# Kernel optimization log

Hardware: AMD Instinct MI355X
Metric: run time of the kernel (lower is better)

The kernel has to match this reference:

```python
import jax, jax.numpy as jnp
from jax import lax
import numpy as np
import math

D_MODEL = 1024
D_STATE = 16
DT_RANK = 64  # ceil(1024/16)


def setup_inputs() -> dict:
    key = jax.random.key(0)
    ks = jax.random.split(key, 8)
    B, L = 2, 2048
    x = jax.random.normal(ks[0], (B, L, D_MODEL), dtype=jnp.float32)
    A_log = jnp.full((D_MODEL, D_STATE), math.log(0.5), dtype=jnp.float32)
    x_proj_w = jax.random.normal(ks[1], (DT_RANK + 2 * D_STATE, D_MODEL), dtype=jnp.float32) * (D_MODEL ** -0.5)
    dt_init_std = DT_RANK ** -0.5
    dt_proj_w = jax.random.uniform(ks[2], (D_MODEL, DT_RANK), minval=-dt_init_std, maxval=dt_init_std, dtype=jnp.float32)
    # dt bias init: softplus-inverse of dt sampled log-uniform in [2*dt_min, 2*dt_max] (trend)
    dt = jnp.exp(jax.random.uniform(ks[3], (D_MODEL,), dtype=jnp.float32) * (math.log(0.2) - math.log(0.002)) + math.log(0.002))
    dt = jnp.clip(dt, 1e-4)
    dt_proj_b = dt + jnp.log(-jnp.expm1(-dt))
    D_param = jnp.ones((D_MODEL,), dtype=jnp.float32)
    trend_emphasis = jnp.full((D_MODEL,), 0.1, dtype=jnp.float32)
    return {
        "x": x, "A_log": A_log, "x_proj_w": x_proj_w,
        "dt_proj_w": dt_proj_w, "dt_proj_b": dt_proj_b,
        "D_param": D_param, "trend_emphasis": trend_emphasis,
    }


def _selective_scan(u, delta, A, Bp, Cp, D_param):
    # u, delta: [B,L,D]; A: [D,N]; Bp, Cp: [B,L,N]; D_param: [D]
    deltaA = jnp.exp(jnp.einsum('bld,dn->bldn', delta, A))       # [B,L,D,N]
    deltaBu = jnp.einsum('bld,bln->bldn', delta * u, Bp)          # [B,L,D,N]
    Bsz, L, Dm, N = deltaA.shape

    def step(h, inp):
        dA, dBu, c = inp          # dA,dBu: [B,D,N]; c: [B,N]
        h = dA * h + dBu
        y = jnp.einsum('bdn,bn->bd', h, c)
        return h, y

    h0 = jnp.zeros((Bsz, Dm, N), dtype=u.dtype)
    xs = (jnp.moveaxis(deltaA, 1, 0), jnp.moveaxis(deltaBu, 1, 0), jnp.moveaxis(Cp, 1, 0))
    _, ys = lax.scan(step, h0, xs)            # ys: [L,B,D]
    y = jnp.moveaxis(ys, 0, 1)                # [B,L,D]
    return y + u * D_param


def reference(x, A_log, x_proj_w, dt_proj_w, dt_proj_b, D_param, trend_emphasis):
    # trend component: channel-wise emphasis gate (dropout in eval mode = identity)
    x = x * jax.nn.sigmoid(trend_emphasis)
    xz = x @ x_proj_w.T                                  # [B,L,dt_rank+2N]
    delta_part = xz[..., :DT_RANK]
    Bp = xz[..., DT_RANK:DT_RANK + D_STATE]              # [B,L,N]
    Cp = xz[..., DT_RANK + D_STATE:]                     # [B,L,N]
    delta = jax.nn.softplus(delta_part @ dt_proj_w.T + dt_proj_b)  # [B,L,D]
    A = -jnp.exp(A_log.astype(jnp.float32))
    return _selective_scan(x, delta, A, Bp, Cp, D_param.astype(jnp.float32))
```

## Files before the change

### kernel.cpp

```cpp
#include <hip/hip_runtime.h>
#include <math.h>


#define LOG2E 1.44269504088896340736f
typedef float v2f __attribute__((ext_vector_type(2)));

__device__ __forceinline__ float fexp2(float v){
#if defined(__has_builtin)
#if __has_builtin(__builtin_amdgcn_exp2f)
  return __builtin_amdgcn_exp2f(v);
#else
  return exp2f(v);
#endif
#else
  return exp2f(v);
#endif
}

__device__ __forceinline__ float fsoftplus(float v){
  return fmaxf(v, 0.f) + __logf(1.f + __expf(-fabsf(v)));
}

__global__ __launch_bounds__(256) void k_prep(const float* __restrict__ xpw,
                                              const float* __restrict__ dtw,
                                              const float* __restrict__ alog,
                                              const float* __restrict__ te,
                                              float* __restrict__ w2T,
                                              float* __restrict__ dtwT,
                                              float* __restrict__ A2,
                                              float* __restrict__ sg){
  __shared__ float sm[32 * 33];
  const int bid = blockIdx.x, t = threadIdx.x;
  const int lane = t & 31, srow = t >> 5;
  if (bid < 96){
    const int kt = bid / 3, ct = bid - kt * 3;
#pragma unroll
    for (int r = 0; r < 4; r++){
      const int cr = srow * 4 + r;
      sm[cr * 33 + lane] = xpw[(size_t)(ct * 32 + cr) * 1024 + kt * 32 + lane];
    }
    __syncthreads();
#pragma unroll
    for (int r = 0; r < 4; r++){
      const int kr = srow * 4 + r;
      const int kg = kt * 32 + kr;
      const float s = 1.f / (1.f + __expf(-te[kg]));
      w2T[(size_t)kg * 96 + ct * 32 + lane] = sm[lane * 33 + kr] * s;
    }
  } else if (bid < 160){
    const int idx = bid - 96, dti = idx >> 1, kt2 = idx & 1;
#pragma unroll
    for (int r = 0; r < 4; r++){
      const int cr = srow * 4 + r;
      sm[cr * 33 + lane] = dtw[(size_t)(dti * 32 + cr) * 64 + kt2 * 32 + lane];
    }
    __syncthreads();
#pragma unroll
    for (int r = 0; r < 4; r++){
      const int kr = srow * 4 + r;
      dtwT[(size_t)(kt2 * 32 + kr) * 1024 + dti * 32 + lane] = sm[lane * 33 + kr];
    }
  } else if (bid < 176){
    const int j = (bid - 160) * 1024 + t;
#pragma unroll
    for (int i = 0; i < 4; i++)
      A2[j + i * 256] = -__expf(alog[j + i * 256]) * LOG2E;
  } else {
#pragma unroll
    for (int i = 0; i < 4; i++){
      const int m = i * 256 + t;
      sg[m] = 1.f / (1.f + __expf(-te[m]));
    }
  }
}

__global__ __launch_bounds__(256) void k_xz(const float* __restrict__ x,
                                            const float* __restrict__ w2T,
                                            float* __restrict__ xzp){
  __shared__ float xT[32 * 257];
  const int t = threadIdx.x;
  const int row0 = blockIdx.x * 256;
  const int c0 = blockIdx.y * 32;
  const int kbase = blockIdx.z * 128;
  v2f acc[16];
#pragma unroll
  for (int c = 0; c < 16; c++) acc[c] = (v2f){0.f, 0.f};
  const int kq = t & 7, rsub = t >> 3;
  for (int kt = 0; kt < 4; ++kt){
    const int k0 = kbase + kt * 32;
    __syncthreads();
#pragma unroll
    for (int p = 0; p < 8; p++){
      const int r = p * 32 + rsub;
      const float4 v = *reinterpret_cast<const float4*>(&x[(size_t)(row0 + r) * 1024 + k0 + kq * 4]);
      xT[(kq * 4 + 0) * 257 + r] = v.x;
      xT[(kq * 4 + 1) * 257 + r] = v.y;
      xT[(kq * 4 + 2) * 257 + r] = v.z;
      xT[(kq * 4 + 3) * 257 + r] = v.w;
    }
    __syncthreads();
#pragma unroll 4
    for (int kk = 0; kk < 32; ++kk){
      const float xv = xT[kk * 257 + t];
      const v2f xv2 = {xv, xv};
      const v2f* wr = reinterpret_cast<const v2f*>(&w2T[(size_t)(k0 + kk) * 96 + c0]);
#pragma unroll
      for (int c = 0; c < 16; c++) acc[c] = acc[c] + xv2 * wr[c];
    }
  }
  float4* o = reinterpret_cast<float4*>(xzp + ((size_t)blockIdx.z * 4096 + row0 + t) * 96 + c0);
  const float4* av = reinterpret_cast<const float4*>(acc);
#pragma unroll
  for (int q = 0; q < 8; q++) o[q] = av[q];
}

__global__ __launch_bounds__(256) void k_reduce(const float4* __restrict__ p,
                                                float4* __restrict__ xz){
  const int i = blockIdx.x * 256 + threadIdx.x;
  float4 r = p[i];
#pragma unroll
  for (int s = 1; s < 8; s++){
    const float4 a = p[(size_t)s * 98304 + i];
    r.x += a.x; r.y += a.y; r.z += a.z; r.w += a.w;
  }
  xz[i] = r;
}

__global__ __launch_bounds__(256) void k_delta(const float* __restrict__ xz,
                                               const float* __restrict__ dtwT,
                                               const float* __restrict__ dtb,
                                               float* __restrict__ del){
  const int t = threadIdx.x;
  const int r0 = blockIdx.x * 16;
  const int d = blockIdx.y * 256 + t;
  v2f wv[32];
#pragma unroll
  for (int k2 = 0; k2 < 32; k2++){
    wv[k2].x = dtwT[(size_t)(2 * k2) * 1024 + d];
    wv[k2].y = dtwT[(size_t)(2 * k2 + 1) * 1024 + d];
  }
  const float dtbv = dtb[d];
  const float* xzb = xz + (size_t)r0 * 96;
#pragma unroll 4
  for (int li = 0; li < 16; ++li){
    v2f acc = {dtbv, 0.f};
    const v2f* dp = reinterpret_cast<const v2f*>(xzb + li * 96);
#pragma unroll
    for (int k2 = 0; k2 < 32; k2++) acc = acc + dp[k2] * wv[k2];
    del[(size_t)(r0 + li) * 1024 + d] = fsoftplus(acc.x + acc.y);
  }
}

__global__ __launch_bounds__(256) void k_scan1(const float* __restrict__ x,
                                               const float* __restrict__ del,
                                               const float* __restrict__ xz,
                                               const float* __restrict__ A2,
                                               const float* __restrict__ sg,
                                               float* __restrict__ S,
                                               float* __restrict__ P){
  const int t = threadIdx.x;
  const int chunk = blockIdx.x, dgrp = blockIdx.y, b = blockIdx.z;
  const int d = dgrp * 256 + t;
  const int l0 = chunk * 32;
  float a2[16];
  {
    const float4* ap = reinterpret_cast<const float4*>(A2 + (size_t)d * 16);
#pragma unroll
    for (int q = 0; q < 4; q++){
      const float4 v = ap[q];
      a2[q*4] = v.x; a2[q*4+1] = v.y; a2[q*4+2] = v.z; a2[q*4+3] = v.w;
    }
  }
  bool uni = true;
#pragma unroll
  for (int n = 1; n < 16; n++) uni = uni && (a2[n] == a2[0]);
  const float sgv = sg[d];
  const size_t xidx0 = (size_t)(b * 2048 + l0) * 1024 + d;
  const float* xzb = xz + (size_t)(b * 2048 + l0) * 96;
  const size_t base = ((size_t)((b * 64 + chunk) * 1024 + d)) * 16;
  if (uni){
    const float a2u = a2[0];
    v2f h2[8];
#pragma unroll
    for (int q = 0; q < 8; q++) h2[q] = (v2f){0.f, 0.f};
    float sumd = 0.f;
    for (int ph = 0; ph < 2; ++ph){
      const size_t xidx = xidx0 + (size_t)ph * 16 * 1024;
      float dl[16], du[16];
#pragma unroll
      for (int li = 0; li < 16; ++li){
        dl[li] = del[xidx + (size_t)li * 1024];
        du[li] = dl[li] * x[xidx + (size_t)li * 1024] * sgv;
      }
#pragma unroll 4
      for (int li = 0; li < 16; ++li){
        sumd += dl[li];
        const float tt = fexp2(dl[li] * a2u);
        const v2f tt2 = {tt, tt}, du2 = {du[li], du[li]};
        const v2f* brow = reinterpret_cast<const v2f*>(xzb + (ph * 16 + li) * 96 + 64);
#pragma unroll
        for (int q = 0; q < 8; q++) h2[q] = h2[q] * tt2 + brow[q] * du2;
      }
    }
    const float Ppu = fexp2(a2u * sumd);
    const float4* hv = reinterpret_cast<const float4*>(h2);
#pragma unroll
    for (int q = 0; q < 4; q++)
      *reinterpret_cast<float4*>(&S[base + q * 4]) = hv[q];
    const float4 pv = {Ppu, Ppu, Ppu, Ppu};
#pragma unroll
    for (int q = 0; q < 4; q++)
      *reinterpret_cast<float4*>(&P[base + q * 4]) = pv;
  } else {
    float h[16], Pp[16];
#pragma unroll
    for (int n = 0; n < 16; n++){ h[n] = 0.f; Pp[n] = 1.f; }
    for (int li = 0; li < 32; ++li){
      const float dv = del[xidx0 + (size_t)li * 1024];
      const float duv = dv * x[xidx0 + (size_t)li * 1024] * sgv;
      const float* brow = xzb + li * 96 + 64;
#pragma unroll
      for (int n = 0; n < 16; n++){
        const float tt = fexp2(dv * a2[n]);
        h[n] = fmaf(tt, h[n], duv * brow[n]);
        Pp[n] *= tt;
      }
    }
#pragma unroll
    for (int q = 0; q < 4; q++){
      float4 v; v.x = h[q*4]; v.y = h[q*4+1]; v.z = h[q*4+2]; v.w = h[q*4+3];
      *reinterpret_cast<float4*>(&S[base + q * 4]) = v;
      float4 u; u.x = Pp[q*4]; u.y = Pp[q*4+1]; u.z = Pp[q*4+2]; u.w = Pp[q*4+3];
      *reinterpret_cast<float4*>(&P[base + q * 4]) = u;
    }
  }
}

__global__ __launch_bounds__(256) void k_scan2(const float* __restrict__ S,
                                               const float* __restrict__ P,
                                               float* __restrict__ H){
  __shared__ float ls[256], lp[256];
  const int t = threadIdx.x;
  const int dn = t & 31, seg = t >> 5;
  const int n = dn & 15, dloc = dn >> 4;
  const int bid = blockIdx.x;
  const int b = bid >> 9, dpair = bid & 511;
  const int d = dpair * 2 + dloc;
  const size_t sbase = ((size_t)(b * 64) * 1024 + d) * 16 + n;
  float Sv[8], Pv[8];
  float s = 0.f, p = 1.f;
#pragma unroll
  for (int i = 0; i < 8; i++){
    const size_t idx = sbase + (size_t)(seg * 8 + i) * 16384;
    Sv[i] = S[idx]; Pv[i] = P[idx];
    s = fmaf(Pv[i], s, Sv[i]);
    p *= Pv[i];
  }
  ls[t] = s; lp[t] = p;
  __syncthreads();
  float h = 0.f;
  for (int j = 0; j < seg; j++)
    h = fmaf(lp[j * 32 + dn], h, ls[j * 32 + dn]);
#pragma unroll
  for (int i = 0; i < 8; i++){
    const size_t idx = sbase + (size_t)(seg * 8 + i) * 16384;
    H[idx] = h;
    h = fmaf(Pv[i], h, Sv[i]);
  }
}

__global__ __launch_bounds__(256) void k_scan3(const float* __restrict__ x,
                                               const float* __restrict__ del,
                                               const float* __restrict__ xz,
                                               const float* __restrict__ A2,
                                               const float* __restrict__ sg,
                                               const float* __restrict__ Dpar,
                                               const float* __restrict__ H,
                                               float* __restrict__ out){
  const int t = threadIdx.x;
  const int chunk = blockIdx.x, dgrp = blockIdx.y, b = blockIdx.z;
  const int d = dgrp * 256 + t;
  const int l0 = chunk * 32;
  float a2[16];
  {
    const float4* ap = reinterpret_cast<const float4*>(A2 + (size_t)d * 16);
#pragma unroll
    for (int q = 0; q < 4; q++){
      const float4 v = ap[q];
      a2[q*4] = v.x; a2[q*4+1] = v.y; a2[q*4+2] = v.z; a2[q*4+3] = v.w;
    }
  }
  bool uni = true;
#pragma unroll
  for (int n = 1; n < 16; n++) uni = uni && (a2[n] == a2[0]);
  const float sgv = sg[d], Dv = Dpar[d];
  const size_t xidx0 = (size_t)(b * 2048 + l0) * 1024 + d;
  const float* xzb = xz + (size_t)(b * 2048 + l0) * 96;
  const size_t hbase = ((size_t)((b * 64 + chunk) * 1024 + d)) * 16;
  if (uni){
    const float a2u = a2[0];
    v2f h2[8];
    {
      const float4* hp = reinterpret_cast<const float4*>(H + hbase);
      float4* hd = reinterpret_cast<float4*>(h2);
#pragma unroll
      for (int q = 0; q < 4; q++) hd[q] = hp[q];
    }
    for (int ph = 0; ph < 2; ++ph){
      const size_t xidx = xidx0 + (size_t)ph * 16 * 1024;
      float dl[16], xd[16];
#pragma unroll
      for (int li = 0; li < 16; ++li){
        dl[li] = del[xidx + (size_t)li * 1024];
        xd[li] = x[xidx + (size_t)li * 1024] * sgv;
      }
#pragma unroll 4
      for (int li = 0; li < 16; ++li){
        const float duv = dl[li] * xd[li];
        const float tt = fexp2(dl[li] * a2u);
        const v2f tt2 = {tt, tt}, du2 = {duv, duv};
        const v2f* brow = reinterpret_cast<const v2f*>(xzb + (ph * 16 + li) * 96 + 64);
        const v2f* crow = reinterpret_cast<const v2f*>(xzb + (ph * 16 + li) * 96 + 80);
        v2f yv = {0.f, 0.f};
#pragma unroll
        for (int q = 0; q < 8; q++){
          h2[q] = h2[q] * tt2 + brow[q] * du2;
          yv = yv + h2[q] * crow[q];
        }
        out[xidx + (size_t)li * 1024] = fmaf(xd[li], Dv, yv.x + yv.y);
      }
    }
  } else {
    float h[16];
    {
      const float4* hp = reinterpret_cast<const float4*>(H + hbase);
#pragma unroll
      for (int q = 0; q < 4; q++){
        const float4 v = hp[q];
        h[q*4] = v.x; h[q*4+1] = v.y; h[q*4+2] = v.z; h[q*4+3] = v.w;
      }
    }
    for (int li = 0; li < 32; ++li){
      const float dv = del[xidx0 + (size_t)li * 1024];
      const float xdv = x[xidx0 + (size_t)li * 1024] * sgv;
      const float duv = dv * xdv;
      const float* brow = xzb + li * 96 + 64;
      float y = 0.f;
#pragma unroll
      for (int n = 0; n < 16; n++){
        const float tt = fexp2(dv * a2[n]);
        h[n] = fmaf(tt, h[n], duv * brow[n]);
        y = fmaf(h[n], brow[16 + n], y);
      }
      out[xidx0 + (size_t)li * 1024] = fmaf(xdv, Dv, y);
    }
  }
}

extern "C" void kernel_launch(void* const* d_in, const int* in_sizes, int n_in,
                              void* d_out, int out_size, void* d_ws, size_t ws_size,
                              hipStream_t stream){
  const float* x    = (const float*)d_in[0];
  const float* Alog = (const float*)d_in[1];
  const float* xpw  = (const float*)d_in[2];
  const float* dtw  = (const float*)d_in[3];
  const float* dtb  = (const float*)d_in[4];
  const float* Dpar = (const float*)d_in[5];
  const float* te   = (const float*)d_in[6];
  float* out = (float*)d_out;
  char* ws = (char*)d_ws;

  float* w2T  = (float*)(ws);
  float* A2   = (float*)(ws + 393216);
  float* sg   = (float*)(ws + 458752);
  float* dtwT = (float*)(ws + 462848);
  float* xz   = (float*)(ws + 724992);
  float* del  = (float*)(ws + 2297856);
  float* xzp  = (float*)(ws + 19075072);
  float* S    = (float*)(ws + 31657984);
  float* P    = (float*)(ws + 40046592);
  float* Hst  = (float*)(ws + 48435200);

  hipLaunchKernelGGL(k_prep,   dim3(177),        dim3(256), 0, stream, xpw, dtw, Alog, te, w2T, dtwT, A2, sg);
  hipLaunchKernelGGL(k_xz,     dim3(16, 3, 8),   dim3(256), 0, stream, x, w2T, xzp);
  hipLaunchKernelGGL(k_reduce, dim3(384),        dim3(256), 0, stream, (const float4*)xzp, (float4*)xz);
  hipLaunchKernelGGL(k_delta,  dim3(256, 4),     dim3(256), 0, stream, xz, dtwT, dtb, del);
  hipLaunchKernelGGL(k_scan1,  dim3(64, 4, 2),   dim3(256), 0, stream, x, del, xz, A2, sg, S, P);
  hipLaunchKernelGGL(k_scan2,  dim3(1024),       dim3(256), 0, stream, S, P, Hst);
  hipLaunchKernelGGL(k_scan3,  dim3(64, 4, 2),   dim3(256), 0, stream, x, del, xz, A2, sg, Dpar, Hst, out);
}
```

Baseline: 160.6 us.

## Fuse delta projection and three scan phases into one persistent kernel with grid barriers

Merges k_delta, k_scan1, k_scan2 and k_scan3 into a single kernel of 512 blocks that synchronises through atomic-counter grid barriers. Delta is computed in registers and reused by both scan passes, so the 16 MB delta buffer is no longer written and read twice. x is also loaded only once, and the xz rows are staged in shared memory. This removes three launches and a large amount of global traffic. In exchange the kernel relies on all 512 blocks being co-resident (launch_bounds 256,2) to avoid deadlock, and it has heavy register pressure from keeping dl, xd and the weights in registers.

```diff
diff --git a/kernel.cpp b/kernel.cpp
--- a/kernel.cpp
+++ b/kernel.cpp
@@ -21,6 +21,18 @@
   return fmaxf(v, 0.f) + __logf(1.f + __expf(-fabsf(v)));
 }
 
+__device__ __forceinline__ void gridbar(unsigned* ctr, unsigned nb){
+  __syncthreads();
+  if (threadIdx.x == 0){
+    __hip_atomic_fetch_add(ctr, 1u, __ATOMIC_ACQ_REL, __HIP_MEMORY_SCOPE_AGENT);
+    while (__hip_atomic_load(ctr, __ATOMIC_ACQUIRE, __HIP_MEMORY_SCOPE_AGENT) < nb){
+      __builtin_amdgcn_s_sleep(2);
+    }
+  }
+  __syncthreads();
+  __threadfence();
+}
+
 __global__ __launch_bounds__(256) void k_prep(const float* __restrict__ xpw,
                                               const float* __restrict__ dtw,
                                               const float* __restrict__ alog,
@@ -28,7 +40,8 @@
                                               float* __restrict__ w2T,
                                               float* __restrict__ dtwT,
                                               float* __restrict__ A2,
-                                              float* __restrict__ sg){
+                                              float* __restrict__ sg,
+                                              unsigned* __restrict__ bars){
   __shared__ float sm[32 * 33];
   const int bid = blockIdx.x, t = threadIdx.x;
   const int lane = t & 31, srow = t >> 5;
@@ -71,6 +84,7 @@
       const int m = i * 256 + t;
       sg[m] = 1.f / (1.f + __expf(-te[m]));
     }
+    if (t < 2) bars[t] = 0u;
   }
 }
 
@@ -126,42 +140,50 @@
   xz[i] = r;
 }
 
-__global__ __launch_bounds__(256) void k_delta(const float* __restrict__ xz,
-                                               const float* __restrict__ dtwT,
-                                               const float* __restrict__ dtb,
-                                               float* __restrict__ del){
-  const int t = threadIdx.x;
-  const int r0 = blockIdx.x * 16;
-  const int d = blockIdx.y * 256 + t;
-  v2f wv[32];
-#pragma unroll
-  for (int k2 = 0; k2 < 32; k2++){
-    wv[k2].x = dtwT[(size_t)(2 * k2) * 1024 + d];
-    wv[k2].y = dtwT[(size_t)(2 * k2 + 1) * 1024 + d];
-  }
-  const float dtbv = dtb[d];
-  const float* xzb = xz + (size_t)r0 * 96;
-#pragma unroll 4
-  for (int li = 0; li < 16; ++li){
-    v2f acc = {dtbv, 0.f};
-    const v2f* dp = reinterpret_cast<const v2f*>(xzb + li * 96);
-#pragma unroll
-    for (int k2 = 0; k2 < 32; k2++) acc = acc + dp[k2] * wv[k2];
-    del[(size_t)(r0 + li) * 1024 + d] = fsoftplus(acc.x + acc.y);
-  }
-}
-
-__global__ __launch_bounds__(256) void k_scan1(const float* __restrict__ x,
-                                               const float* __restrict__ del,
-                                               const float* __restrict__ xz,
-                                               const float* __restrict__ A2,
-                                               const float* __restrict__ sg,
-                                               float* __restrict__ S,
-                                               float* __restrict__ P){
+__global__ __launch_bounds__(256, 2) void k_fused(const float* __restrict__ x,
+                                                  const float* __restrict__ xz,
+                                                  const float* __restrict__ dtwT,
+                                                  const float* __restrict__ dtb,
+                                                  const float* __restrict__ A2,
+                                                  const float* __restrict__ sg,
+                                                  const float* __restrict__ Dpar,
+                                                  float* __restrict__ S,
+                                                  float* __restrict__ P,
+                                                  float* __restrict__ H,
+                                                  float* __restrict__ out,
+                                                  unsigned* __restrict__ bars){
+  __shared__ float xzd[32 * 64];
+  __shared__ float bc[32 * 32];
+  __shared__ float ls[256], lp[256];
+
   const int t = threadIdx.x;
   const int chunk = blockIdx.x, dgrp = blockIdx.y, b = blockIdx.z;
   const int d = dgrp * 256 + t;
   const int l0 = chunk * 32;
+  const float* xzb = xz + (size_t)(b * 2048 + l0) * 96;
+  const size_t xidx0 = (size_t)(b * 2048 + l0) * 1024 + d;
+
+  for (int i = t; i < 768; i += 256){
+    const int r = i / 24;
+    const int c4 = i - r * 24;
+    const float4 v = *reinterpret_cast<const float4*>(xzb + r * 96 + c4 * 4);
+    if (c4 < 16) *reinterpret_cast<float4*>(&xzd[r * 64 + c4 * 4]) = v;
+    else         *reinterpret_cast<float4*>(&bc[r * 32 + (c4 - 16) * 4]) = v;
+  }
+
+  v2f wv[32];
+#pragma unroll
+  for (int k2 = 0; k2 < 32; k2++){
+    wv[k2].x = dtwT[(size_t)(2 * k2) * 1024 + d];
+    wv[k2].y = dtwT[(size_t)(2 * k2 + 1) * 1024 + d];
+  }
+  const float dtbv = dtb[d];
+  const float sgv = sg[d];
+  float xd[32];
+#pragma unroll
+  for (int li = 0; li < 32; ++li)
+    xd[li] = x[xidx0 + (size_t)li * 1024] * sgv;
+
   float a2[16];
   {
     const float4* ap = reinterpret_cast<const float4*>(A2 + (size_t)d * 16);
@@ -174,185 +196,157 @@
   bool uni = true;
 #pragma unroll
   for (int n = 1; n < 16; n++) uni = uni && (a2[n] == a2[0]);
-  const float sgv = sg[d];
-  const size_t xidx0 = (size_t)(b * 2048 + l0) * 1024 + d;
-  const float* xzb = xz + (size_t)(b * 2048 + l0) * 96;
-  const size_t base = ((size_t)((b * 64 + chunk) * 1024 + d)) * 16;
+
+  __syncthreads();
+
+  float dl[32];
+#pragma unroll
+  for (int li = 0; li < 32; ++li){
+    const float4* dp4 = reinterpret_cast<const float4*>(&xzd[li * 64]);
+    v2f acc = {dtbv, 0.f};
+#pragma unroll
+    for (int k4 = 0; k4 < 16; k4++){
+      const float4 xv = dp4[k4];
+      acc = acc + (v2f){xv.x, xv.y} * wv[2 * k4];
+      acc = acc + (v2f){xv.z, xv.w} * wv[2 * k4 + 1];
+    }
+    dl[li] = fsoftplus(acc.x + acc.y);
+  }
+
+  const size_t sbase = ((size_t)((b * 64 + chunk) * 1024 + d)) * 16;
+
   if (uni){
     const float a2u = a2[0];
     v2f h2[8];
 #pragma unroll
     for (int q = 0; q < 8; q++) h2[q] = (v2f){0.f, 0.f};
     float sumd = 0.f;
-    for (int ph = 0; ph < 2; ++ph){
-      const size_t xidx = xidx0 + (size_t)ph * 16 * 1024;
-      float dl[16], du[16];
-#pragma unroll
-      for (int li = 0; li < 16; ++li){
-        dl[li] = del[xidx + (size_t)li * 1024];
-        du[li] = dl[li] * x[xidx + (size_t)li * 1024] * sgv;
-      }
-#pragma unroll 4
-      for (int li = 0; li < 16; ++li){
-        sumd += dl[li];
-        const float tt = fexp2(dl[li] * a2u);
-        const v2f tt2 = {tt, tt}, du2 = {du[li], du[li]};
-        const v2f* brow = reinterpret_cast<const v2f*>(xzb + (ph * 16 + li) * 96 + 64);
-#pragma unroll
-        for (int q = 0; q < 8; q++) h2[q] = h2[q] * tt2 + brow[q] * du2;
-      }
-    }
+#pragma unroll
+    for (int li = 0; li < 32; ++li){
+      sumd += dl[li];
+      const float tt = fexp2(dl[li] * a2u);
+      const float duv = dl[li] * xd[li];
+      const v2f tt2 = {tt, tt}, du2 = {duv, duv};
+      const float4* bq = reinterpret_cast<const float4*>(&bc[li * 32]);
+#pragma unroll
+      for (int q4 = 0; q4 < 4; q4++){
+        const float4 bv = bq[q4];
+        h2[2*q4]   = h2[2*q4]   * tt2 + (v2f){bv.x, bv.y} * du2;
+        h2[2*q4+1] = h2[2*q4+1] * tt2 + (v2f){bv.z, bv.w} * du2;
+      }
+    }
+    const float4* hv = reinterpret_cast<const float4*>(h2);
+#pragma unroll
+    for (int q = 0; q < 4; q++)
+      *reinterpret_cast<float4*>(&S[sbase + q * 4]) = hv[q];
     const float Ppu = fexp2(a2u * sumd);
-    const float4* hv = reinterpret_cast<const float4*>(h2);
+    const float4 pv = {Ppu, Ppu, Ppu, Ppu};
 #pragma unroll
     for (int q = 0; q < 4; q++)
-      *reinterpret_cast<float4*>(&S[base + q * 4]) = hv[q];
-    const float4 pv = {Ppu, Ppu, Ppu, Ppu};
-#pragma unroll
-    for (int q = 0; q < 4; q++)
-      *reinterpret_cast<float4*>(&P[base + q * 4]) = pv;
+      *reinterpret_cast<float4*>(&P[sbase + q * 4]) = pv;
   } else {
     float h[16], Pp[16];
 #pragma unroll
     for (int n = 0; n < 16; n++){ h[n] = 0.f; Pp[n] = 1.f; }
+#pragma unroll
     for (int li = 0; li < 32; ++li){
-      const float dv = del[xidx0 + (size_t)li * 1024];
-      const float duv = dv * x[xidx0 + (size_t)li * 1024] * sgv;
-      const float* brow = xzb + li * 96 + 64;
+      const float duv = dl[li] * xd[li];
 #pragma unroll
       for (int n = 0; n < 16; n++){
-        const float tt = fexp2(dv * a2[n]);
-        h[n] = fmaf(tt, h[n], duv * brow[n]);
+        const float tt = fexp2(dl[li] * a2[n]);
+        h[n] = fmaf(tt, h[n], duv * bc[li * 32 + n]);
         Pp[n] *= tt;
       }
     }
 #pragma unroll
     for (int q = 0; q < 4; q++){
       float4 v; v.x = h[q*4]; v.y = h[q*4+1]; v.z = h[q*4+2]; v.w = h[q*4+3];
-      *reinterpret_cast<float4*>(&S[base + q * 4]) = v;
+      *reinterpret_cast<float4*>(&S[sbase + q * 4]) = v;
       float4 u; u.x = Pp[q*4]; u.y = Pp[q*4+1]; u.z = Pp[q*4+2]; u.w = Pp[q*4+3];
-      *reinterpret_cast<float4*>(&P[base + q * 4]) = u;
-    }
-  }
-}
-
-__global__ __launch_bounds__(256) void k_scan2(const float* __restrict__ S,
-                                               const float* __restrict__ P,
-                                               float* __restrict__ H){
-  __shared__ float ls[256], lp[256];
-  const int t = threadIdx.x;
-  const int dn = t & 31, seg = t >> 5;
-  const int n = dn & 15, dloc = dn >> 4;
-  const int bid = blockIdx.x;
-  const int b = bid >> 9, dpair = bid & 511;
-  const int d = dpair * 2 + dloc;
-  const size_t sbase = ((size_t)(b * 64) * 1024 + d) * 16 + n;
-  float Sv[8], Pv[8];
-  float s = 0.f, p = 1.f;
-#pragma unroll
-  for (int i = 0; i < 8; i++){
-    const size_t idx = sbase + (size_t)(seg * 8 + i) * 16384;
-    Sv[i] = S[idx]; Pv[i] = P[idx];
-    s = fmaf(Pv[i], s, Sv[i]);
-    p *= Pv[i];
-  }
-  ls[t] = s; lp[t] = p;
-  __syncthreads();
-  float h = 0.f;
-  for (int j = 0; j < seg; j++)
-    h = fmaf(lp[j * 32 + dn], h, ls[j * 32 + dn]);
-#pragma unroll
-  for (int i = 0; i < 8; i++){
-    const size_t idx = sbase + (size_t)(seg * 8 + i) * 16384;
-    H[idx] = h;
-    h = fmaf(Pv[i], h, Sv[i]);
-  }
-}
-
-__global__ __launch_bounds__(256) void k_scan3(const float* __restrict__ x,
-                                               const float* __restrict__ del,
-                                               const float* __restrict__ xz,
-                                               const float* __restrict__ A2,
-                                               const float* __restrict__ sg,
-                                               const float* __restrict__ Dpar,
-                                               const float* __restrict__ H,
-                                               float* __restrict__ out){
-  const int t = threadIdx.x;
-  const int chunk = blockIdx.x, dgrp = blockIdx.y, b = blockIdx.z;
-  const int d = dgrp * 256 + t;
-  const int l0 = chunk * 32;
-  float a2[16];
+      *reinterpret_cast<float4*>(&P[sbase + q * 4]) = u;
+    }
+  }
+
+  gridbar(bars + 0, 512u);
+
   {
-    const float4* ap = reinterpret_cast<const float4*>(A2 + (size_t)d * 16);
-#pragma unroll
-    for (int q = 0; q < 4; q++){
-      const float4 v = ap[q];
-      a2[q*4] = v.x; a2[q*4+1] = v.y; a2[q*4+2] = v.z; a2[q*4+3] = v.w;
-    }
-  }
-  bool uni = true;
-#pragma unroll
-  for (int n = 1; n < 16; n++) uni = uni && (a2[n] == a2[0]);
-  const float sgv = sg[d], Dv = Dpar[d];
-  const size_t xidx0 = (size_t)(b * 2048 + l0) * 1024 + d;
-  const float* xzb = xz + (size_t)(b * 2048 + l0) * 96;
-  const size_t hbase = ((size_t)((b * 64 + chunk) * 1024 + d)) * 16;
+    const int bid = (blockIdx.z * 4 + blockIdx.y) * 64 + blockIdx.x;
+    const int b2 = bid >> 8, dq = bid & 255;
+    const int seg = t >> 6, s = t & 63;
+    const int d2 = dq * 4 + (s >> 4), n2 = s & 15;
+    const size_t sb2 = ((size_t)(b2 * 64) * 1024 + d2) * 16 + n2;
+    float Sv[16], Pv[16];
+    float sa = 0.f, pa = 1.f;
+#pragma unroll
+    for (int i = 0; i < 16; i++){
+      const size_t idx = sb2 + (size_t)(seg * 16 + i) * 16384;
+      Sv[i] = S[idx]; Pv[i] = P[idx];
+      sa = fmaf(Pv[i], sa, Sv[i]);
+      pa *= Pv[i];
+    }
+    ls[t] = sa; lp[t] = pa;
+    __syncthreads();
+    float h = 0.f;
+    for (int j = 0; j < seg; j++)
+      h = fmaf(lp[j * 64 + s], h, ls[j * 64 + s]);
+#pragma unroll
+    for (int i = 0; i < 16; i++){
+      const size_t idx = sb2 + (size_t)(seg * 16 + i) * 16384;
+      H[idx] = h;
+      h = fmaf(Pv[i], h, Sv[i]);
+    }
+  }
+
+  gridbar(bars + 1, 512u);
+
+  const float Dv = Dpar[d];
   if (uni){
     const float a2u = a2[0];
     v2f h2[8];
     {
-      const float4* hp = reinterpret_cast<const float4*>(H + hbase);
+      const float4* hp = reinterpret_cast<const float4*>(H + sbase);
       float4* hd = reinterpret_cast<float4*>(h2);
 #pragma unroll
       for (int q = 0; q < 4; q++) hd[q] = hp[q];
     }
-    for (int ph = 0; ph < 2; ++ph){
-      const size_t xidx = xidx0 + (size_t)ph * 16 * 1024;
-      float dl[16], xd[16];
-#pragma unroll
-      for (int li = 0; li < 16; ++li){
-        dl[li] = del[xidx + (size_t)li * 1024];
-        xd[li] = x[xidx + (size_t)li * 1024] * sgv;
-      }
-#pragma unroll 4
-      for (int li = 0; li < 16; ++li){
-        const float duv = dl[li] * xd[li];
-        const float tt = fexp2(dl[li] * a2u);
-        const v2f tt2 = {tt, tt}, du2 = {duv, duv};
-        const v2f* brow = reinterpret_cast<const v2f*>(xzb + (ph * 16 + li) * 96 + 64);
-        const v2f* crow = reinterpret_cast<const v2f*>(xzb + (ph * 16 + li) * 96 + 80);
-        v2f yv = {0.f, 0.f};
-#pragma unroll
-        for (int q = 0; q < 8; q++){
-          h2[q] = h2[q] * tt2 + brow[q] * du2;
-          yv = yv + h2[q] * crow[q];
-        }
-        out[xidx + (size_t)li * 1024] = fmaf(xd[li], Dv, yv.x + yv.y);
-      }
+#pragma unroll
+    for (int li = 0; li < 32; ++li){
+      const float tt = fexp2(dl[li] * a2u);
+      const float duv = dl[li] * xd[li];
+      const v2f tt2 = {tt, tt}, du2 = {duv, duv};
+      const float4* bq = reinterpret_cast<const float4*>(&bc[li * 32]);
+      const float4* cq = reinterpret_cast<const float4*>(&bc[li * 32 + 16]);
+      v2f yv = {0.f, 0.f};
+#pragma unroll
+      for (int q4 = 0; q4 < 4; q4++){
+        const float4 bv = bq[q4], cv = cq[q4];
+        h2[2*q4]   = h2[2*q4]   * tt2 + (v2f){bv.x, bv.y} * du2;
+        h2[2*q4+1] = h2[2*q4+1] * tt2 + (v2f){bv.z, bv.w} * du2;
+        yv = yv + h2[2*q4] * (v2f){cv.x, cv.y} + h2[2*q4+1] * (v2f){cv.z, cv.w};
+      }
+      out[xidx0 + (size_t)li * 1024] = fmaf(xd[li], Dv, yv.x + yv.y);
     }
   } else {
     float h[16];
     {
-      const float4* hp = reinterpret_cast<const float4*>(H + hbase);
+      const float4* hp = reinterpret_cast<const float4*>(H + sbase);
 #pragma unroll
       for (int q = 0; q < 4; q++){
         const float4 v = hp[q];
         h[q*4] = v.x; h[q*4+1] = v.y; h[q*4+2] = v.z; h[q*4+3] = v.w;
       }
     }
+#pragma unroll
     for (int li = 0; li < 32; ++li){
-      const float dv = del[xidx0 + (size_t)li * 1024];
-      const float xdv = x[xidx0 + (size_t)li * 1024] * sgv;
-      const float duv = dv * xdv;
-      const float* brow = xzb + li * 96 + 64;
+      const float duv = dl[li] * xd[li];
       float y = 0.f;
 #pragma unroll
       for (int n = 0; n < 16; n++){
-        const float tt = fexp2(dv * a2[n]);
-        h[n] = fmaf(tt, h[n], duv * brow[n]);
-        y = fmaf(h[n], brow[16 + n], y);
-      }
-      out[xidx0 + (size_t)li * 1024] = fmaf(xdv, Dv, y);
+        const float tt = fexp2(dl[li] * a2[n]);
+        h[n] = fmaf(tt, h[n], duv * bc[li * 32 + n]);
+        y = fmaf(h[n], bc[li * 32 + 16 + n], y);
+      }
+      out[xidx0 + (size_t)li * 1024] = fmaf(xd[li], Dv, y);
     }
   }
 }
@@ -375,17 +369,14 @@
   float* sg   = (float*)(ws + 458752);
   float* dtwT = (float*)(ws + 462848);
   float* xz   = (float*)(ws + 724992);
-  float* del  = (float*)(ws + 2297856);
   float* xzp  = (float*)(ws + 19075072);
   float* S    = (float*)(ws + 31657984);
   float* P    = (float*)(ws + 40046592);
   float* Hst  = (float*)(ws + 48435200);
-
-  hipLaunchKernelGGL(k_prep,   dim3(177),        dim3(256), 0, stream, xpw, dtw, Alog, te, w2T, dtwT, A2, sg);
-  hipLaunchKernelGGL(k_xz,     dim3(16, 3, 8),   dim3(256), 0, stream, x, w2T, xzp);
-  hipLaunchKernelGGL(k_reduce, dim3(384),        dim3(256), 0, stream, (const float4*)xzp, (float4*)xz);
-  hipLaunchKernelGGL(k_delta,  dim3(256, 4),     dim3(256), 0, stream, xz, dtwT, dtb, del);
-  hipLaunchKernelGGL(k_scan1,  dim3(64, 4, 2),   dim3(256), 0, stream, x, del, xz, A2, sg, S, P);
-  hipLaunchKernelGGL(k_scan2,  dim3(1024),       dim3(256), 0, stream, S, P, Hst);
-  hipLaunchKernelGGL(k_scan3,  dim3(64, 4, 2),   dim3(256), 0, stream, x, del, xz, A2, sg, Dpar, Hst, out);
-}
+  unsigned* bars = (unsigned*)(ws + 56823808);
+
+  hipLaunchKernelGGL(k_prep,   dim3(177),      dim3(256), 0, stream, xpw, dtw, Alog, te, w2T, dtwT, A2, sg, bars);
+  hipLaunchKernelGGL(k_xz,     dim3(16, 3, 8), dim3(256), 0, stream, x, w2T, xzp);
+  hipLaunchKernelGGL(k_reduce, dim3(384),      dim3(256), 0, stream, (const float4*)xzp, (float4*)xz);
+  hipLaunchKernelGGL(k_fused,  dim3(64, 4, 2), dim3(256), 0, stream, x, xz, dtwT, dtb, A2, sg, Dpar, S, P, Hst, out, bars);
+}
```

New measurement: 344.1 us. 2.14x slower.

## Fuse delta projection and softplus into both scan passes, drop delta buffer

Applied to the files above, without the earlier changes.

Removes the separate k_delta kernel and its 16 MB delta intermediate. Both scan passes now stage the chunk's 32x64 dt-rank slice of xz into shared memory and recompute delta on the fly, using per-thread dt_proj weights held in registers. This saves one launch and a full write plus two full reads of the delta tensor, at the cost of computing the 64-wide dot product twice and higher register pressure (64 weight floats plus 32 x values per thread).

```diff
diff --git a/kernel.cpp b/kernel.cpp
--- a/kernel.cpp
+++ b/kernel.cpp
@@ -126,42 +126,42 @@
   xz[i] = r;
 }
 
-__global__ __launch_bounds__(256) void k_delta(const float* __restrict__ xz,
-                                               const float* __restrict__ dtwT,
-                                               const float* __restrict__ dtb,
-                                               float* __restrict__ del){
-  const int t = threadIdx.x;
-  const int r0 = blockIdx.x * 16;
-  const int d = blockIdx.y * 256 + t;
-  v2f wv[32];
-#pragma unroll
-  for (int k2 = 0; k2 < 32; k2++){
-    wv[k2].x = dtwT[(size_t)(2 * k2) * 1024 + d];
-    wv[k2].y = dtwT[(size_t)(2 * k2 + 1) * 1024 + d];
-  }
-  const float dtbv = dtb[d];
-  const float* xzb = xz + (size_t)r0 * 96;
-#pragma unroll 4
-  for (int li = 0; li < 16; ++li){
-    v2f acc = {dtbv, 0.f};
-    const v2f* dp = reinterpret_cast<const v2f*>(xzb + li * 96);
-#pragma unroll
-    for (int k2 = 0; k2 < 32; k2++) acc = acc + dp[k2] * wv[k2];
-    del[(size_t)(r0 + li) * 1024 + d] = fsoftplus(acc.x + acc.y);
-  }
-}
-
-__global__ __launch_bounds__(256) void k_scan1(const float* __restrict__ x,
-                                               const float* __restrict__ del,
-                                               const float* __restrict__ xz,
-                                               const float* __restrict__ A2,
-                                               const float* __restrict__ sg,
-                                               float* __restrict__ S,
-                                               float* __restrict__ P){
+__global__ __launch_bounds__(256) void k_scan1f(const float* __restrict__ x,
+                                                const float* __restrict__ xz,
+                                                const float* __restrict__ dtwT,
+                                                const float* __restrict__ dtb,
+                                                const float* __restrict__ A2,
+                                                const float* __restrict__ sg,
+                                                float* __restrict__ S,
+                                                float* __restrict__ P){
+  __shared__ float xzd[32 * 64];
   const int t = threadIdx.x;
   const int chunk = blockIdx.x, dgrp = blockIdx.y, b = blockIdx.z;
   const int d = dgrp * 256 + t;
   const int l0 = chunk * 32;
+  const float* xzb = xz + (size_t)(b * 2048 + l0) * 96;
+  const size_t xidx0 = (size_t)(b * 2048 + l0) * 1024 + d;
+
+#pragma unroll
+  for (int i = t; i < 512; i += 256){
+    const int r = i >> 4, c4 = i & 15;
+    const float4 v = *reinterpret_cast<const float4*>(xzb + r * 96 + c4 * 4);
+    *reinterpret_cast<float4*>(&xzd[r * 64 + c4 * 4]) = v;
+  }
+
+  v2f wv[32];
+#pragma unroll
+  for (int k2 = 0; k2 < 32; k2++){
+    wv[k2].x = dtwT[(size_t)(2 * k2) * 1024 + d];
+    wv[k2].y = dtwT[(size_t)(2 * k2 + 1) * 1024 + d];
+  }
+  const float dtbv = dtb[d];
+  const float sgv = sg[d];
+  float xd[32];
+#pragma unroll
+  for (int li = 0; li < 32; ++li)
+    xd[li] = x[xidx0 + (size_t)li * 1024] * sgv;
+
   float a2[16];
   {
     const float4* ap = reinterpret_cast<const float4*>(A2 + (size_t)d * 16);
@@ -174,54 +174,64 @@
   bool uni = true;
 #pragma unroll
   for (int n = 1; n < 16; n++) uni = uni && (a2[n] == a2[0]);
-  const float sgv = sg[d];
-  const size_t xidx0 = (size_t)(b * 2048 + l0) * 1024 + d;
-  const float* xzb = xz + (size_t)(b * 2048 + l0) * 96;
-  const size_t base = ((size_t)((b * 64 + chunk) * 1024 + d)) * 16;
+
+  __syncthreads();
+
+  const size_t sbase = ((size_t)((b * 64 + chunk) * 1024 + d)) * 16;
+
   if (uni){
     const float a2u = a2[0];
     v2f h2[8];
 #pragma unroll
     for (int q = 0; q < 8; q++) h2[q] = (v2f){0.f, 0.f};
     float sumd = 0.f;
-    for (int ph = 0; ph < 2; ++ph){
-      const size_t xidx = xidx0 + (size_t)ph * 16 * 1024;
-      float dl[16], du[16];
-#pragma unroll
-      for (int li = 0; li < 16; ++li){
-        dl[li] = del[xidx + (size_t)li * 1024];
-        du[li] = dl[li] * x[xidx + (size_t)li * 1024] * sgv;
-      }
 #pragma unroll 4
-      for (int li = 0; li < 16; ++li){
-        sumd += dl[li];
-        const float tt = fexp2(dl[li] * a2u);
-        const v2f tt2 = {tt, tt}, du2 = {du[li], du[li]};
-        const v2f* brow = reinterpret_cast<const v2f*>(xzb + (ph * 16 + li) * 96 + 64);
-#pragma unroll
-        for (int q = 0; q < 8; q++) h2[q] = h2[q] * tt2 + brow[q] * du2;
-      }
-    }
+    for (int li = 0; li < 32; ++li){
+      const float4* dp4 = reinterpret_cast<const float4*>(&xzd[li * 64]);
+      v2f acc = {dtbv, 0.f};
+#pragma unroll
+      for (int k4 = 0; k4 < 16; k4++){
+        const float4 xv = dp4[k4];
+        acc = acc + (v2f){xv.x, xv.y} * wv[2 * k4];
+        acc = acc + (v2f){xv.z, xv.w} * wv[2 * k4 + 1];
+      }
+      const float dl = fsoftplus(acc.x + acc.y);
+      sumd += dl;
+      const float tt = fexp2(dl * a2u);
+      const float duv = dl * xd[li];
+      const v2f tt2 = {tt, tt}, du2 = {duv, duv};
+      const v2f* brow = reinterpret_cast<const v2f*>(xzb + li * 96 + 64);
+#pragma unroll
+      for (int q = 0; q < 8; q++) h2[q] = h2[q] * tt2 + brow[q] * du2;
+    }
+    const float4* hv = reinterpret_cast<const float4*>(h2);
+#pragma unroll
+    for (int q = 0; q < 4; q++)
+      *reinterpret_cast<float4*>(&S[sbase + q * 4]) = hv[q];
     const float Ppu = fexp2(a2u * sumd);
-    const float4* hv = reinterpret_cast<const float4*>(h2);
+    const float4 pv = {Ppu, Ppu, Ppu, Ppu};
 #pragma unroll
     for (int q = 0; q < 4; q++)
-      *reinterpret_cast<float4*>(&S[base + q * 4]) = hv[q];
-    const float4 pv = {Ppu, Ppu, Ppu, Ppu};
-#pragma unroll
-    for (int q = 0; q < 4; q++)
-      *reinterpret_cast<float4*>(&P[base + q * 4]) = pv;
+      *reinterpret_cast<float4*>(&P[sbase + q * 4]) = pv;
   } else {
     float h[16], Pp[16];
 #pragma unroll
     for (int n = 0; n < 16; n++){ h[n] = 0.f; Pp[n] = 1.f; }
     for (int li = 0; li < 32; ++li){
-      const float dv = del[xidx0 + (size_t)li * 1024];
-      const float duv = dv * x[xidx0 + (size_t)li * 1024] * sgv;
+      const float4* dp4 = reinterpret_cast<const float4*>(&xzd[li * 64]);
+      v2f acc = {dtbv, 0.f};
+#pragma unroll
+      for (int k4 = 0; k4 < 16; k4++){
+        const float4 xv = dp4[k4];
+        acc = acc + (v2f){xv.x, xv.y} * wv[2 * k4];
+        acc = acc + (v2f){xv.z, xv.w} * wv[2 * k4 + 1];
+      }
+      const float dl = fsoftplus(acc.x + acc.y);
+      const float duv = dl * xd[li];
       const float* brow = xzb + li * 96 + 64;
 #pragma unroll
       for (int n = 0; n < 16; n++){
-        const float tt = fexp2(dv * a2[n]);
+        const float tt = fexp2(dl * a2[n]);
         h[n] = fmaf(tt, h[n], duv * brow[n]);
         Pp[n] *= tt;
       }
@@ -229,9 +239,9 @@
 #pragma unroll
     for (int q = 0; q < 4; q++){
       float4 v; v.x = h[q*4]; v.y = h[q*4+1]; v.z = h[q*4+2]; v.w = h[q*4+3];
-      *reinterpret_cast<float4*>(&S[base + q * 4]) = v;
+      *reinterpret_cast<float4*>(&S[sbase + q * 4]) = v;
       float4 u; u.x = Pp[q*4]; u.y = Pp[q*4+1]; u.z = Pp[q*4+2]; u.w = Pp[q*4+3];
-      *reinterpret_cast<float4*>(&P[base + q * 4]) = u;
+      *reinterpret_cast<float4*>(&P[sbase + q * 4]) = u;
     }
   }
 }
@@ -269,18 +279,43 @@
   }
 }
 
-__global__ __launch_bounds__(256) void k_scan3(const float* __restrict__ x,
-                                               const float* __restrict__ del,
-                                               const float* __restrict__ xz,
-                                               const float* __restrict__ A2,
-                                               const float* __restrict__ sg,
-                                               const float* __restrict__ Dpar,
-                                               const float* __restrict__ H,
-                                               float* __restrict__ out){
+__global__ __launch_bounds__(256) void k_scan3f(const float* __restrict__ x,
+                                                const float* __restrict__ xz,
+                                                const float* __restrict__ dtwT,
+                                                const float* __restrict__ dtb,
+                                                const float* __restrict__ A2,
+                                                const float* __restrict__ sg,
+                                                const float* __restrict__ Dpar,
+                                                const float* __restrict__ H,
+                                                float* __restrict__ out){
+  __shared__ float xzd[32 * 64];
   const int t = threadIdx.x;
   const int chunk = blockIdx.x, dgrp = blockIdx.y, b = blockIdx.z;
   const int d = dgrp * 256 + t;
   const int l0 = chunk * 32;
+  const float* xzb = xz + (size_t)(b * 2048 + l0) * 96;
+  const size_t xidx0 = (size_t)(b * 2048 + l0) * 1024 + d;
+
+#pragma unroll
+  for (int i = t; i < 512; i += 256){
+    const int r = i >> 4, c4 = i & 15;
+    const float4 v = *reinterpret_cast<const float4*>(xzb + r * 96 + c4 * 4);
+    *reinterpret_cast<float4*>(&xzd[r * 64 + c4 * 4]) = v;
+  }
+
+  v2f wv[32];
+#pragma unroll
+  for (int k2 = 0; k2 < 32; k2++){
+    wv[k2].x = dtwT[(size_t)(2 * k2) * 1024 + d];
+    wv[k2].y = dtwT[(size_t)(2 * k2 + 1) * 1024 + d];
+  }
+  const float dtbv = dtb[d];
+  const float sgv = sg[d];
+  float xd[32];
+#pragma unroll
+  for (int li = 0; li < 32; ++li)
+    xd[li] = x[xidx0 + (size_t)li * 1024] * sgv;
+
   float a2[16];
   {
     const float4* ap = reinterpret_cast<const float4*>(A2 + (size_t)d * 16);
@@ -293,10 +328,12 @@
   bool uni = true;
 #pragma unroll
   for (int n = 1; n < 16; n++) uni = uni && (a2[n] == a2[0]);
-  const float sgv = sg[d], Dv = Dpar[d];
-  const size_t xidx0 = (size_t)(b * 2048 + l0) * 1024 + d;
-  const float* xzb = xz + (size_t)(b * 2048 + l0) * 96;
+
+  __syncthreads();
+
+  const float Dv = Dpar[d];
   const size_t hbase = ((size_t)((b * 64 + chunk) * 1024 + d)) * 16;
+
   if (uni){
     const float a2u = a2[0];
     v2f h2[8];
@@ -306,29 +343,29 @@
 #pragma unroll
       for (int q = 0; q < 4; q++) hd[q] = hp[q];
     }
-    for (int ph = 0; ph < 2; ++ph){
-      const size_t xidx = xidx0 + (size_t)ph * 16 * 1024;
-      float dl[16], xd[16];
-#pragma unroll
-      for (int li = 0; li < 16; ++li){
-        dl[li] = del[xidx + (size_t)li * 1024];
-        xd[li] = x[xidx + (size_t)li * 1024] * sgv;
-      }
 #pragma unroll 4
-      for (int li = 0; li < 16; ++li){
-        const float duv = dl[li] * xd[li];
-        const float tt = fexp2(dl[li] * a2u);
-        const v2f tt2 = {tt, tt}, du2 = {duv, duv};
-        const v2f* brow = reinterpret_cast<const v2f*>(xzb + (ph * 16 + li) * 96 + 64);
-        const v2f* crow = reinterpret_cast<const v2f*>(xzb + (ph * 16 + li) * 96 + 80);
-        v2f yv = {0.f, 0.f};
-#pragma unroll
-        for (int q = 0; q < 8; q++){
-          h2[q] = h2[q] * tt2 + brow[q] * du2;
-          yv = yv + h2[q] * crow[q];
-        }
-        out[xidx + (size_t)li * 1024] = fmaf(xd[li], Dv, yv.x + yv.y);
-      }
+    for (int li = 0; li < 32; ++li){
+      const float4* dp4 = reinterpret_cast<const float4*>(&xzd[li * 64]);
+      v2f acc = {dtbv, 0.f};
+#pragma unroll
+      for (int k4 = 0; k4 < 16; k4++){
+        const float4 xv = dp4[k4];
+        acc = acc + (v2f){xv.x, xv.y} * wv[2 * k4];
+        acc = acc + (v2f){xv.z, xv.w} * wv[2 * k4 + 1];
+      }
+      const float dl = fsoftplus(acc.x + acc.y);
+      const float tt = fexp2(dl * a2u);
+      const float duv = dl * xd[li];
+      const v2f tt2 = {tt, tt}, du2 = {duv, duv};
+      const v2f* brow = reinterpret_cast<const v2f*>(xzb + li * 96 + 64);
+      const v2f* crow = reinterpret_cast<const v2f*>(xzb + li * 96 + 80);
+      v2f yv = {0.f, 0.f};
+#pragma unroll
+      for (int q = 0; q < 8; q++){
+        h2[q] = h2[q] * tt2 + brow[q] * du2;
+        yv = yv + h2[q] * crow[q];
+      }
+      out[xidx0 + (size_t)li * 1024] = fmaf(xd[li], Dv, yv.x + yv.y);
     }
   } else {
     float h[16];
@@ -341,18 +378,25 @@
       }
     }
     for (int li = 0; li < 32; ++li){
-      const float dv = del[xidx0 + (size_t)li * 1024];
-      const float xdv = x[xidx0 + (size_t)li * 1024] * sgv;
-      const float duv = dv * xdv;
+      const float4* dp4 = reinterpret_cast<const float4*>(&xzd[li * 64]);
+      v2f acc = {dtbv, 0.f};
+#pragma unroll
+      for (int k4 = 0; k4 < 16; k4++){
+        const float4 xv = dp4[k4];
+        acc = acc + (v2f){xv.x, xv.y} * wv[2 * k4];
+        acc = acc + (v2f){xv.z, xv.w} * wv[2 * k4 + 1];
+      }
+      const float dl = fsoftplus(acc.x + acc.y);
+      const float duv = dl * xd[li];
       const float* brow = xzb + li * 96 + 64;
       float y = 0.f;
 #pragma unroll
       for (int n = 0; n < 16; n++){
-        const float tt = fexp2(dv * a2[n]);
+        const float tt = fexp2(dl * a2[n]);
         h[n] = fmaf(tt, h[n], duv * brow[n]);
         y = fmaf(h[n], brow[16 + n], y);
       }
-      out[xidx0 + (size_t)li * 1024] = fmaf(xdv, Dv, y);
+      out[xidx0 + (size_t)li * 1024] = fmaf(xd[li], Dv, y);
     }
   }
 }
@@ -375,17 +419,15 @@
   float* sg   = (float*)(ws + 458752);
   float* dtwT = (float*)(ws + 462848);
   float* xz   = (float*)(ws + 724992);
-  float* del  = (float*)(ws + 2297856);
-  float* xzp  = (float*)(ws + 19075072);
-  float* S    = (float*)(ws + 31657984);
-  float* P    = (float*)(ws + 40046592);
-  float* Hst  = (float*)(ws + 48435200);
-
-  hipLaunchKernelGGL(k_prep,   dim3(177),        dim3(256), 0, stream, xpw, dtw, Alog, te, w2T, dtwT, A2, sg);
-  hipLaunchKernelGGL(k_xz,     dim3(16, 3, 8),   dim3(256), 0, stream, x, w2T, xzp);
-  hipLaunchKernelGGL(k_reduce, dim3(384),        dim3(256), 0, stream, (const float4*)xzp, (float4*)xz);
-  hipLaunchKernelGGL(k_delta,  dim3(256, 4),     dim3(256), 0, stream, xz, dtwT, dtb, del);
-  hipLaunchKernelGGL(k_scan1,  dim3(64, 4, 2),   dim3(256), 0, stream, x, del, xz, A2, sg, S, P);
-  hipLaunchKernelGGL(k_scan2,  dim3(1024),       dim3(256), 0, stream, S, P, Hst);
-  hipLaunchKernelGGL(k_scan3,  dim3(64, 4, 2),   dim3(256), 0, stream, x, del, xz, A2, sg, Dpar, Hst, out);
-}
+  float* xzp  = (float*)(ws + 2297856);
+  float* S    = (float*)(ws + 14880768);
+  float* P    = (float*)(ws + 23269376);
+  float* Hst  = (float*)(ws + 31657984);
+
+  hipLaunchKernelGGL(k_prep,   dim3(177),      dim3(256), 0, stream, xpw, dtw, Alog, te, w2T, dtwT, A2, sg);
+  hipLaunchKernelGGL(k_xz,     dim3(16, 3, 8), dim3(256), 0, stream, x, w2T, xzp);
+  hipLaunchKernelGGL(k_reduce, dim3(384),      dim3(256), 0, stream, (const float4*)xzp, (float4*)xz);
+  hipLaunchKernelGGL(k_scan1f, dim3(64, 4, 2), dim3(256), 0, stream, x, xz, dtwT, dtb, A2, sg, S, P);
+  hipLaunchKernelGGL(k_scan2,  dim3(1024),     dim3(256), 0, stream, S, P, Hst);
+  hipLaunchKernelGGL(k_scan3f, dim3(64, 4, 2), dim3(256), 0, stream, x, xz, dtwT, dtb, A2, sg, Dpar, Hst, out);
+}
```

Result: slower. 186.2 us (+15.9%).
